# Kernel tuning notes

Measured on AMD Instinct MI355X. Metric: run time of the kernel, lower is better.

Reference implementation:

```python
import jax, jax.numpy as jnp
import numpy as np

NUM_HEADS = 8
DIM_HEAD = 64
GROUPS = 32
EPS = 1e-5


def setup_inputs() -> dict:
    key = jax.random.key(0)
    k1, k2, k3 = jax.random.split(key, 3)
    C = 512
    inner = NUM_HEADS * DIM_HEAD  # 512
    x = jax.random.normal(k1, (8, C, 32, 32), dtype=jnp.float32)
    gamma = jnp.ones((C,), dtype=jnp.float32)
    beta = jnp.zeros((C,), dtype=jnp.float32)
    w_qkv = jax.random.normal(k2, (3 * inner, C), dtype=jnp.float32) * 0.02
    w_out = jax.random.normal(k3, (C, inner), dtype=jnp.float32) * 0.02
    return {"x": x, "gamma": gamma, "beta": beta, "w_qkv": w_qkv, "w_out": w_out}


def group_norm(x, gamma, beta):
    b, c, h, w = x.shape
    xg = x.reshape(b, GROUPS, c // GROUPS, h, w)
    mean = jnp.mean(xg, axis=(2, 3, 4), keepdims=True)
    var = jnp.var(xg, axis=(2, 3, 4), keepdims=True)
    xn = ((xg - mean) * jax.lax.rsqrt(var + EPS)).reshape(b, c, h, w)
    return xn * gamma[None, :, None, None] + beta[None, :, None, None]


def reference(x, gamma, beta, w_qkv, w_out):
    b, c, h, w = x.shape
    H, d = NUM_HEADS, DIM_HEAD
    inner = H * d
    scale = d ** (-0.5)
    residual = x
    xn = group_norm(x, gamma, beta)
    # 1x1 conv (no bias) == channel matmul
    qkv = jnp.einsum('bchw,oc->bohw', xn, w_qkv)  # [b, 3*inner, h, w]
    q, k, v = jnp.split(qkv, 3, axis=1)
    def to_heads(t):
        # b (H d) h w -> b H (h w) d
        return t.reshape(b, H, d, h * w).transpose(0, 1, 3, 2)
    q, k, v = to_heads(q), to_heads(k), to_heads(v)
    attn = jnp.einsum('bhid,bhjd->bhij', q, k) * scale  # [b,H,hw,hw]
    attn = jax.nn.softmax(attn, axis=-1)
    out = jnp.einsum('bhij,bhjd->bhid', attn, v)  # [b,H,hw,d]
    # b H (h w) d -> b (H d) h w
    out = out.transpose(0, 1, 3, 2).reshape(b, inner, h, w)
    out = jnp.einsum('bchw,oc->bohw', out, w_out)
    return out + residual
```

## Files before the change

kernel.cpp:

```cpp
#include <hip/hip_runtime.h>


typedef __attribute__((ext_vector_type(8))) short bf16x8;
typedef __attribute__((ext_vector_type(4))) short bf16x4;
typedef __attribute__((ext_vector_type(4))) float f32x4;
typedef __attribute__((ext_vector_type(16))) float f32x16;

#define NB 8
#define NC 512
#define HW 1024
#define NHEAD 8
#define DHEAD 64
#define GROUPS 32
#define CPG 16
#define QKV_N 1536

#define GLL16(gaddr, ldsaddr)                                                  \
    __builtin_amdgcn_global_load_lds(                                          \
        (const __attribute__((address_space(1))) unsigned*)(gaddr),            \
        (__attribute__((address_space(3))) unsigned*)(ldsaddr), 16, 0, 0)

__device__ alignas(64) short g_xn[(size_t)8192 * 512];
__device__ alignas(64) short g_qkv[(size_t)8192 * 1536];
__device__ alignas(64) short g_vt[(size_t)64 * 64 * 1024];
__device__ alignas(64) short g_attno[(size_t)8192 * 512];
__device__ alignas(64) short g_wqkv[(size_t)1536 * 512];
__device__ alignas(64) short g_wout[(size_t)512 * 512];

__device__ __forceinline__ float b2f(short h) {
    union { unsigned u; float f; } v;
    v.u = ((unsigned)(unsigned short)h) << 16;
    return v.f;
}
__device__ __forceinline__ short f2b(float f) {
    union { float f; unsigned u; } v;
    v.f = f;
    unsigned r = v.u + 0x7fff + ((v.u >> 16) & 1);
    return (short)(r >> 16);
}

__global__ __launch_bounds__(256) void prep_kernel(
    const float* __restrict__ x, const float* __restrict__ gamma,
    const float* __restrict__ beta, const float* __restrict__ wqkv,
    const float* __restrict__ wout) {
    int tid = threadIdx.x;
    if (blockIdx.x >= 256) {
        int wb = blockIdx.x - 256;
        for (int i = wb * 256 + tid; i < 1536 * 512; i += 64 * 256) {
            float v = wqkv[i];
            if (i < 512 * 512) v *= 0.18033688011112042f;
            g_wqkv[i] = f2b(v);
        }
        for (int i = wb * 256 + tid; i < 512 * 512; i += 64 * 256)
            g_wout[i] = f2b(wout[i]);
        return;
    }
    int b = blockIdx.x >> 5, g = blockIdx.x & 31;
    __shared__ alignas(16) short tile[CPG][HW];
    __shared__ float red[2][4];
    __shared__ float sg[CPG], sb[CPG];
    if (tid < CPG) {
        int cg = g * CPG + tid;
        sg[tid] = gamma[cg];
        sb[tid] = beta[cg];
    }
    const float* xb = x + (size_t)b * NC * HW + (size_t)g * CPG * HW;
    float s1 = 0.f, s2 = 0.f;
    #pragma unroll
    for (int it = 0; it < 8; it++) {
        int idx = tid + it * 256;
        f32x4 v0 = *(const f32x4*)(xb + idx * 8);
        f32x4 v1 = *(const f32x4*)(xb + idx * 8 + 4);
        bf16x8 w;
        #pragma unroll
        for (int j = 0; j < 4; j++) {
            s1 += v0[j] + v1[j]; s2 += v0[j] * v0[j] + v1[j] * v1[j];
            w[j] = f2b(v0[j]); w[j + 4] = f2b(v1[j]);
        }
        *(bf16x8*)(&((short*)tile)[idx * 8]) = w;
    }
    #pragma unroll
    for (int off = 32; off; off >>= 1) { s1 += __shfl_xor(s1, off); s2 += __shfl_xor(s2, off); }
    int wid = tid >> 6;
    if ((tid & 63) == 0) { red[0][wid] = s1; red[1][wid] = s2; }
    __syncthreads();
    float t1 = red[0][0] + red[0][1] + red[0][2] + red[0][3];
    float t2 = red[1][0] + red[1][1] + red[1][2] + red[1][3];
    float mean = t1 * (1.f / 16384.f);
    float var  = t2 * (1.f / 16384.f) - mean * mean;
    float inv  = rsqrtf(var + 1e-5f);
    #pragma unroll
    for (int p = 0; p < 4; p++) {
        int s = tid * 4 + p;
        bf16x8 pk0, pk1;
        #pragma unroll
        for (int cc = 0; cc < 8; cc++) {
            pk0[cc] = f2b((b2f(tile[cc][s])     - mean) * inv * sg[cc]     + sb[cc]);
            pk1[cc] = f2b((b2f(tile[cc + 8][s]) - mean) * inv * sg[cc + 8] + sb[cc + 8]);
        }
        size_t dst = ((size_t)(b * HW + s)) * NC + g * CPG;
        *(bf16x8*)(g_xn + dst)     = pk0;
        *(bf16x8*)(g_xn + dst + 8) = pk1;
    }
}

__global__ __launch_bounds__(256) void gemm_qkv() {
    const int K = NC;
    int tid = threadIdx.x, lane = tid & 63, wid = tid >> 6;
    int quad = lane >> 4, l15 = lane & 15;
    int row0 = blockIdx.x * 128;
    int col0 = blockIdx.y * 128;
    __shared__ alignas(16) short sa[128 * 64];
    __shared__ alignas(16) short sbuf[128 * 64];
    int r_lo = lane >> 3;
    int s_log = (lane & 7) ^ r_lo;
    int swz = l15 & 7;
    const short* ga = g_xn   + (size_t)(row0 + wid * 32 + r_lo) * K + s_log * 8;
    const short* gb = g_wqkv + (size_t)(col0 + wid * 32 + r_lo) * K + s_log * 8;
    int mw = (wid >> 1) * 64, nw = (wid & 1) * 64;
    f32x4 acc[4][4] = {};
    for (int k = 0; k < K; k += 64) {
        #pragma unroll
        for (int c = 0; c < 4; c++) {
            GLL16(ga + (size_t)(c * 8) * K + k, &sa[(wid * 32 + c * 8) * 64]);
            GLL16(gb + (size_t)(c * 8) * K + k, &sbuf[(wid * 32 + c * 8) * 64]);
        }
        __syncthreads();
        bf16x8 af0[4], af1[4], bf0[4], bf1[4];
        #pragma unroll
        for (int m = 0; m < 4; m++) {
            int row = mw + m * 16 + l15;
            af0[m] = *(const bf16x8*)&sa[row * 64 + ((quad ^ swz) * 8)];
            af1[m] = *(const bf16x8*)&sa[row * 64 + (((4 + quad) ^ swz) * 8)];
        }
        #pragma unroll
        for (int n = 0; n < 4; n++) {
            int row = nw + n * 16 + l15;
            bf0[n] = *(const bf16x8*)&sbuf[row * 64 + ((quad ^ swz) * 8)];
            bf1[n] = *(const bf16x8*)&sbuf[row * 64 + (((4 + quad) ^ swz) * 8)];
        }
        #pragma unroll
        for (int m = 0; m < 4; m++)
            #pragma unroll
            for (int n = 0; n < 4; n++) {
                acc[m][n] = __builtin_amdgcn_mfma_f32_16x16x32_bf16(af0[m], bf0[n], acc[m][n], 0, 0, 0);
                acc[m][n] = __builtin_amdgcn_mfma_f32_16x16x32_bf16(af1[m], bf1[n], acc[m][n], 0, 0, 0);
            }
        __syncthreads();
    }
    #pragma unroll
    for (int m = 0; m < 4; m++)
        #pragma unroll
        for (int n = 0; n < 4; n++)
            #pragma unroll
            for (int r = 0; r < 4; r++) {
                int row = row0 + mw + m * 16 + quad * 4 + r;
                int col = col0 + nw + n * 16 + l15;
                g_qkv[(size_t)row * QKV_N + col] = f2b(acc[m][n][r]);
            }
}

__global__ __launch_bounds__(256) void transpose_v() {
    int bh = blockIdx.x & 63, st = blockIdx.x >> 6;
    int b = bh >> 3, h = bh & 7;
    int tid = threadIdx.x;
    __shared__ alignas(16) short tile[64][72];
    int s0 = st * 64;
    #pragma unroll
    for (int cc = 0; cc < 2; cc++) {
        int idx = tid + cc * 256;
        int s = idx >> 3, dc = idx & 7;
        *(bf16x8*)&tile[s][dc * 8] =
            *(const bf16x8*)(g_qkv + ((size_t)(b * HW + s0 + s)) * QKV_N + 1024 + h * DHEAD + dc * 8);
    }
    __syncthreads();
    #pragma unroll
    for (int cc = 0; cc < 2; cc++) {
        int idx = tid + cc * 256;
        int d = idx & 63, sc = idx >> 6;
        bf16x8 o;
        #pragma unroll
        for (int j = 0; j < 8; j++) o[j] = tile[sc * 8 + j][d];
        *(bf16x8*)(g_vt + ((size_t)(bh * 64 + d)) * HW + s0 + sc * 8) = o;
    }
}

__global__ __launch_bounds__(256) void attn_kernel() {
    int bh = blockIdx.x & 63, qt = blockIdx.x >> 6;
    int b = bh >> 3, h = bh & 7;
    int tid = threadIdx.x, lane = tid & 63, wid = tid >> 6;
    int l31 = lane & 31, hl = lane >> 5;
    __shared__ alignas(16) short kt[2][64 * 64];
    __shared__ alignas(16) short vt[2][64 * 64];
    int qrow0 = qt * 128 + wid * 32;

    const short* qb = g_qkv + ((size_t)(b * HW + qrow0 + l31)) * QKV_N + h * DHEAD + hl * 8;
    bf16x8 aq[4];
    #pragma unroll
    for (int ks = 0; ks < 4; ks++) aq[ks] = *(const bf16x8*)(qb + ks * 16);

    f32x16 acc_o0 = {}, acc_o1 = {}, acc_l = {};
    bf16x8 vone;
    #pragma unroll
    for (int j = 0; j < 8; j++) vone[j] = (short)0x3f80;

    int r_lo = lane >> 3;
    int s_log = (lane & 7) ^ r_lo;

    auto stage = [&](int it, int bufi) {
        int t0 = it * 64;
        #pragma unroll
        for (int c = 0; c < 2; c++) {
            int r = wid * 16 + c * 8 + r_lo;
            GLL16(g_qkv + ((size_t)(b * HW + t0 + r)) * QKV_N + 512 + h * DHEAD + s_log * 8,
                  &kt[bufi][(wid * 16 + c * 8) * 64]);
            GLL16(g_vt + ((size_t)(bh * 64 + r)) * HW + t0 + s_log * 8,
                  &vt[bufi][(wid * 16 + c * 8) * 64]);
        }
    };

    stage(0, 0);
    __syncthreads();
    for (int it = 0; it < 16; it++) {
        int cur = it & 1;
        if (it < 15) stage(it + 1, cur ^ 1);
        f32x16 z0 = {}, z1 = {};
        #pragma unroll
        for (int ks = 0; ks < 4; ks++) {
            int g0 = ks * 2 + hl;
            int rowa = l31;
            bf16x8 k0 = *(const bf16x8*)&kt[cur][rowa * 64 + ((g0 ^ (rowa & 7)) * 8)];
            z0 = __builtin_amdgcn_mfma_f32_32x32x16_bf16(k0, aq[ks], z0, 0, 0, 0);
            int rowb = 32 + l31;
            bf16x8 k1 = *(const bf16x8*)&kt[cur][rowb * 64 + ((g0 ^ (rowb & 7)) * 8)];
            z1 = __builtin_amdgcn_mfma_f32_32x32x16_bf16(k1, aq[ks], z1, 0, 0, 0);
        }
        unsigned u0[8], u1[8];
        #pragma unroll
        for (int p = 0; p < 8; p++) {
            float e0, e1, e2, e3;
            asm("v_exp_f32 %0, %1" : "=v"(e0) : "v"(z0[2 * p]));
            asm("v_exp_f32 %0, %1" : "=v"(e1) : "v"(z0[2 * p + 1]));
            asm("v_exp_f32 %0, %1" : "=v"(e2) : "v"(z1[2 * p]));
            asm("v_exp_f32 %0, %1" : "=v"(e3) : "v"(z1[2 * p + 1]));
            asm("v_cvt_pk_bf16_f32 %0, %1, %2" : "=v"(u0[p]) : "v"(e0), "v"(e1));
            asm("v_cvt_pk_bf16_f32 %0, %1, %2" : "=v"(u1[p]) : "v"(e2), "v"(e3));
        }
        bf16x8 ap[4];
        #pragma unroll
        for (int th = 0; th < 2; th++) {
            #pragma unroll
            for (int ks1 = 0; ks1 < 2; ks1++) {
                unsigned x0 = th ? u1[4 * ks1]     : u0[4 * ks1];
                unsigned y0 = th ? u1[4 * ks1 + 2] : u0[4 * ks1 + 2];
                unsigned x1 = th ? u1[4 * ks1 + 1] : u0[4 * ks1 + 1];
                unsigned y1 = th ? u1[4 * ks1 + 3] : u0[4 * ks1 + 3];
                asm("v_permlane32_swap_b32 %0, %1" : "+v"(x0), "+v"(y0));
                asm("v_permlane32_swap_b32 %0, %1" : "+v"(x1), "+v"(y1));
                union { unsigned w[4]; bf16x8 v; } pa;
                pa.w[0] = x0; pa.w[1] = x1; pa.w[2] = y0; pa.w[3] = y1;
                ap[th * 2 + ks1] = pa.v;
            }
        }
        #pragma unroll
        for (int ks = 0; ks < 4; ks++)
            acc_l = __builtin_amdgcn_mfma_f32_32x32x16_bf16(ap[ks], vone, acc_l, 0, 0, 0);
        #pragma unroll
        for (int ks = 0; ks < 4; ks++) {
            int gt = ks * 2 + hl;
            int rowd0 = l31;
            bf16x8 bv0 = *(const bf16x8*)&vt[cur][rowd0 * 64 + ((gt ^ (rowd0 & 7)) * 8)];
            acc_o0 = __builtin_amdgcn_mfma_f32_32x32x16_bf16(ap[ks], bv0, acc_o0, 0, 0, 0);
            int rowd1 = 32 + l31;
            bf16x8 bv1 = *(const bf16x8*)&vt[cur][rowd1 * 64 + ((gt ^ (rowd1 & 7)) * 8)];
            acc_o1 = __builtin_amdgcn_mfma_f32_32x32x16_bf16(ap[ks], bv1, acc_o1, 0, 0, 0);
        }
        __syncthreads();
    }
    #pragma unroll
    for (int r = 0; r < 16; r++) {
        int m = (r & 3) + 8 * (r >> 2) + 4 * hl;
        float invl = 1.f / acc_l[r];
        size_t row = (size_t)(b * HW + qrow0 + m);
        g_attno[row * NC + h * DHEAD + l31]      = f2b(acc_o0[r] * invl);
        g_attno[row * NC + h * DHEAD + 32 + l31] = f2b(acc_o1[r] * invl);
    }
}

__global__ __launch_bounds__(256) void gemm_out(
    const float* __restrict__ xres, float* __restrict__ out) {
    const int K = NC;
    int tid = threadIdx.x, lane = tid & 63, wid = tid >> 6;
    int quad = lane >> 4, l15 = lane & 15;
    int row0 = blockIdx.x * 128;
    int col0 = blockIdx.y * 128;
    __shared__ alignas(16) short sa[128 * 32];
    __shared__ alignas(16) short sbuf[128 * 32];
    int srow = wid * 32 + (lane >> 2);
    int scol = (lane & 3) * 8;
    const short* ga = g_wout  + (size_t)(row0 + srow) * K + scol;
    const short* gb = g_attno + (size_t)(col0 + srow) * K + scol;
    short* la = sa   + wid * 1024;
    short* lb = sbuf + wid * 1024;
    int mw = (wid >> 1) * 64, nw = (wid & 1) * 64;
    f32x4 acc[4][4] = {};
    for (int k = 0; k < K; k += 32) {
        GLL16(ga + k, la);
        GLL16(ga + (size_t)16 * K + k, la + 512);
        GLL16(gb + k, lb);
        GLL16(gb + (size_t)16 * K + k, lb + 512);
        __syncthreads();
        bf16x8 af[4], bfv[4];
        #pragma unroll
        for (int m = 0; m < 4; m++) af[m]  = *(const bf16x8*)&sa[(mw + m * 16 + l15) * 32 + quad * 8];
        #pragma unroll
        for (int n = 0; n < 4; n++) bfv[n] = *(const bf16x8*)&sbuf[(nw + n * 16 + l15) * 32 + quad * 8];
        #pragma unroll
        for (int m = 0; m < 4; m++)
            #pragma unroll
            for (int n = 0; n < 4; n++)
                acc[m][n] = __builtin_amdgcn_mfma_f32_16x16x32_bf16(af[m], bfv[n], acc[m][n], 0, 0, 0);
        __syncthreads();
    }
    #pragma unroll
    for (int m = 0; m < 4; m++)
        #pragma unroll
        for (int n = 0; n < 4; n++)
            #pragma unroll
            for (int r = 0; r < 4; r++) {
                int o  = row0 + mw + m * 16 + quad * 4 + r;
                int bs = col0 + nw + n * 16 + l15;
                size_t addr = (size_t)(bs >> 10) * ((size_t)NC * HW) + (size_t)o * HW + (bs & 1023);
                out[addr] = acc[m][n][r] + xres[addr];
            }
}

extern "C" void kernel_launch(void* const* d_in, const int* in_sizes, int n_in,
                              void* d_out, int out_size, void* d_ws, size_t ws_size,
                              hipStream_t stream) {
    const float* x     = (const float*)d_in[0];
    const float* gamma = (const float*)d_in[1];
    const float* beta  = (const float*)d_in[2];
    const float* wqkv  = (const float*)d_in[3];
    const float* wout  = (const float*)d_in[4];
    float* out = (float*)d_out;

    prep_kernel<<<dim3(320), dim3(256), 0, stream>>>(x, gamma, beta, wqkv, wout);
    gemm_qkv<<<dim3(64, 12), dim3(256), 0, stream>>>();
    transpose_v<<<dim3(1024), dim3(256), 0, stream>>>();
    attn_kernel<<<dim3(512), dim3(256), 0, stream>>>();
    gemm_out<<<dim3(4, 64), dim3(256), 0, stream>>>(x, out);
}
```

Baseline: 154.9 us.

## Software-pipeline attention loop: overlap next QK/exp with current PV MFMAs

Restructures the attention inner loop so the QK product and exp/pack for tile it+1 are computed while the PV and row-sum MFMAs for tile it are issued. The loads are prefetched two stages ahead, and V fragments are read into registers before the barrier so that buffer can be refilled early. The goal is to hide exp/transcendental latency and LDS waits behind MFMA work. The cost is more live registers (extra ap and bv fragments), which may lower occupancy or cause spills.

```diff
diff --git a/kernel.cpp b/kernel.cpp
--- a/kernel.cpp
+++ b/kernel.cpp
@@ -219,22 +219,20 @@
         }
     };
 
-    stage(0, 0);
-    __syncthreads();
-    for (int it = 0; it < 16; it++) {
-        int cur = it & 1;
-        if (it < 15) stage(it + 1, cur ^ 1);
-        f32x16 z0 = {}, z1 = {};
+    auto qk = [&](int buf, f32x16& z0, f32x16& z1) {
         #pragma unroll
         for (int ks = 0; ks < 4; ks++) {
             int g0 = ks * 2 + hl;
             int rowa = l31;
-            bf16x8 k0 = *(const bf16x8*)&kt[cur][rowa * 64 + ((g0 ^ (rowa & 7)) * 8)];
+            bf16x8 k0 = *(const bf16x8*)&kt[buf][rowa * 64 + ((g0 ^ (rowa & 7)) * 8)];
             z0 = __builtin_amdgcn_mfma_f32_32x32x16_bf16(k0, aq[ks], z0, 0, 0, 0);
             int rowb = 32 + l31;
-            bf16x8 k1 = *(const bf16x8*)&kt[cur][rowb * 64 + ((g0 ^ (rowb & 7)) * 8)];
+            bf16x8 k1 = *(const bf16x8*)&kt[buf][rowb * 64 + ((g0 ^ (rowb & 7)) * 8)];
             z1 = __builtin_amdgcn_mfma_f32_32x32x16_bf16(k1, aq[ks], z1, 0, 0, 0);
         }
+    };
+
+    auto exppack = [&](const f32x16& z0, const f32x16& z1, bf16x8* ap) {
         unsigned u0[8], u1[8];
         #pragma unroll
         for (int p = 0; p < 8; p++) {
@@ -246,7 +244,6 @@
             asm("v_cvt_pk_bf16_f32 %0, %1, %2" : "=v"(u0[p]) : "v"(e0), "v"(e1));
             asm("v_cvt_pk_bf16_f32 %0, %1, %2" : "=v"(u1[p]) : "v"(e2), "v"(e3));
         }
-        bf16x8 ap[4];
         #pragma unroll
         for (int th = 0; th < 2; th++) {
             #pragma unroll
@@ -262,20 +259,60 @@
                 ap[th * 2 + ks1] = pa.v;
             }
         }
-        #pragma unroll
-        for (int ks = 0; ks < 4; ks++)
-            acc_l = __builtin_amdgcn_mfma_f32_32x32x16_bf16(ap[ks], vone, acc_l, 0, 0, 0);
+    };
+
+    stage(0, 0);
+    __syncthreads();
+    stage(1, 1);
+    bf16x8 ap_cur[4];
+    {
+        f32x16 z0 = {}, z1 = {};
+        qk(0, z0, z1);
+        exppack(z0, z1, ap_cur);
+    }
+
+    for (int it = 0; it < 15; it++) {
+        int cur = it & 1, alt = cur ^ 1;
+        bf16x8 bv0[4], bv1[4];
         #pragma unroll
         for (int ks = 0; ks < 4; ks++) {
             int gt = ks * 2 + hl;
             int rowd0 = l31;
-            bf16x8 bv0 = *(const bf16x8*)&vt[cur][rowd0 * 64 + ((gt ^ (rowd0 & 7)) * 8)];
-            acc_o0 = __builtin_amdgcn_mfma_f32_32x32x16_bf16(ap[ks], bv0, acc_o0, 0, 0, 0);
+            bv0[ks] = *(const bf16x8*)&vt[cur][rowd0 * 64 + ((gt ^ (rowd0 & 7)) * 8)];
             int rowd1 = 32 + l31;
-            bf16x8 bv1 = *(const bf16x8*)&vt[cur][rowd1 * 64 + ((gt ^ (rowd1 & 7)) * 8)];
-            acc_o1 = __builtin_amdgcn_mfma_f32_32x32x16_bf16(ap[ks], bv1, acc_o1, 0, 0, 0);
-        }
-        __syncthreads();
+            bv1[ks] = *(const bf16x8*)&vt[cur][rowd1 * 64 + ((gt ^ (rowd1 & 7)) * 8)];
+        }
+        __syncthreads();
+        if (it < 14) stage(it + 2, cur);
+        f32x16 z0 = {}, z1 = {};
+        qk(alt, z0, z1);
+        bf16x8 ap_next[4];
+        exppack(z0, z1, ap_next);
+        #pragma unroll
+        for (int ks = 0; ks < 4; ks++)
+            acc_l = __builtin_amdgcn_mfma_f32_32x32x16_bf16(ap_cur[ks], vone, acc_l, 0, 0, 0);
+        #pragma unroll
+        for (int ks = 0; ks < 4; ks++) {
+            acc_o0 = __builtin_amdgcn_mfma_f32_32x32x16_bf16(ap_cur[ks], bv0[ks], acc_o0, 0, 0, 0);
+            acc_o1 = __builtin_amdgcn_mfma_f32_32x32x16_bf16(ap_cur[ks], bv1[ks], acc_o1, 0, 0, 0);
+        }
+        #pragma unroll
+        for (int ks = 0; ks < 4; ks++) ap_cur[ks] = ap_next[ks];
+    }
+    {
+        #pragma unroll
+        for (int ks = 0; ks < 4; ks++)
+            acc_l = __builtin_amdgcn_mfma_f32_32x32x16_bf16(ap_cur[ks], vone, acc_l, 0, 0, 0);
+        #pragma unroll
+        for (int ks = 0; ks < 4; ks++) {
+            int gt = ks * 2 + hl;
+            int rowd0 = l31;
+            bf16x8 bv0 = *(const bf16x8*)&vt[1][rowd0 * 64 + ((gt ^ (rowd0 & 7)) * 8)];
+            acc_o0 = __builtin_amdgcn_mfma_f32_32x32x16_bf16(ap_cur[ks], bv0, acc_o0, 0, 0, 0);
+            int rowd1 = 32 + l31;
+            bf16x8 bv1 = *(const bf16x8*)&vt[1][rowd1 * 64 + ((gt ^ (rowd1 & 7)) * 8)];
+            acc_o1 = __builtin_amdgcn_mfma_f32_32x32x16_bf16(ap_cur[ks], bv1, acc_o1, 0, 0, 0);
+        }
     }
     #pragma unroll
     for (int r = 0; r < 16; r++) {
```

Measured after the change: 151.8 us (median of 2 runs). 2.0% less time.
